# Kernel optimization log

Hardware: AMD Instinct MI355X
Metric: run time of the kernel (lower is better)

The kernel has to match this reference:

```python
import jax, jax.numpy as jnp
import numpy as np

B, T, D = 1024, 256, 256
H, L, K = 768, 6, 10          # hidden_dim, levels, conv_size
CH = H // L                   # chunk_size
GDIM = 4 * H + 2 * L          # gate projection width


def setup_inputs() -> dict:
    key = jax.random.key(0)
    ks = jax.random.split(key, 10)
    s = lambda n: 1.0 / np.sqrt(n).astype(np.float32)
    return {
        "x": jax.random.normal(ks[0], (B, T, D), jnp.float32),
        "time": jax.random.uniform(ks[1], (B, T), jnp.float32),
        "kernel_w": jax.random.normal(ks[2], (GDIM, D + 1), jnp.float32) * s(D + 1),
        "kernel_b": jnp.zeros((GDIM,), jnp.float32),
        "rec_w": jax.random.normal(ks[3], (GDIM, H + 1), jnp.float32) * s(H + 1),
        "rec_b": jnp.zeros((GDIM,), jnp.float32),
        "scale_w": jax.random.normal(ks[4], (H // 6, H), jnp.float32) * s(H),
        "scale_b": jnp.zeros((H // 6,), jnp.float32),
        "rescale_w": jax.random.normal(ks[5], (H, H // 6), jnp.float32) * s(H // 6),
        "rescale_b": jnp.zeros((H,), jnp.float32),
        "conv_w": jax.random.normal(ks[6], (H, H, K), jnp.float32) * s(H * K),
        "conv_b": jnp.zeros((H,), jnp.float32),
        "out_w": jax.random.normal(ks[7], (1, H), jnp.float32) * s(H),
        "out_b": jnp.zeros((1,), jnp.float32),
    }


def _cumax_l2r(v):
    return jnp.cumsum(jax.nn.softmax(v, axis=-1), axis=-1)


def _cumax_r2l(v):
    v = jnp.flip(v, -1)
    v = jnp.cumsum(jax.nn.softmax(v, axis=-1), axis=-1)
    return jnp.flip(v, -1)


def reference(x, time, kernel_w, kernel_b, rec_w, rec_b, scale_w, scale_b,
              rescale_w, rescale_b, conv_w, conv_b, out_w, out_b):
    b = x.shape[0]

    def step(carry, xs):
        c, h, tmp_h, tmp_dis = carry
        x_t, t_t = xs                              # [b,D], [b]
        xi = jnp.concatenate([x_t, t_t[:, None]], -1)
        hi = jnp.concatenate([h, t_t[:, None]], -1)
        g = xi @ kernel_w.T + kernel_b + hi @ rec_w.T + rec_b   # [b, 4H+2L]
        f_m = _cumax_l2r(g[:, :L])[:, :, None]                  # [b,L,1]
        i_m = _cumax_r2l(g[:, L:2 * L])[:, :, None]             # [b,L,1]
        rest = g[:, 2 * L:].reshape(b, 4 * L, CH)
        f_g = jax.nn.sigmoid(rest[:, :L])
        i_g = jax.nn.sigmoid(rest[:, L:2 * L])
        o_g = jax.nn.sigmoid(rest[:, 2 * L:3 * L])
        c_in = jnp.tanh(rest[:, 3 * L:])
        c_last = c.reshape(b, L, CH)
        ov = f_m * i_m
        c_new3 = ov * (f_g * c_last + i_g * c_in) + (f_m - ov) * c_last + (i_m - ov) * c_in
        h_new = (o_g * jnp.tanh(c_new3)).reshape(b, H)
        c_new = c_new3.reshape(b, H)
        dist = 1.0 - jnp.mean(f_m[..., 0], axis=-1)             # [b]
        tmp_h = jnp.concatenate([tmp_h[1:], h_new[None]], 0)    # sliding window [K,b,H]
        tmp_dis = jnp.concatenate([tmp_dis[1:], dist[None]], 0) # [K,b]
        return (c_new, h_new, tmp_h, tmp_dis), dist

    init = (jnp.zeros((b, H), x.dtype), jnp.zeros((b, H), x.dtype),
            jnp.zeros((K, b, H), x.dtype), jnp.zeros((K, b), x.dtype))
    xs = (jnp.transpose(x, (1, 0, 2)), time.T)
    (c_f, h_last, tmp_h, tmp_dis), distance = jax.lax.scan(step, init, xs)

    local_dis = jax.nn.softmax(jnp.cumsum(tmp_dis.T, axis=1), axis=1)    # [b,K]
    local_h = jnp.transpose(tmp_h, (1, 2, 0)) * local_dis[:, None, :]    # [b,H,K]
    theme = jax.nn.sigmoid(
        jax.nn.relu(jnp.mean(local_h, -1) @ scale_w.T + scale_b) @ rescale_w.T + rescale_b)
    conv = jnp.einsum('bhk,ohk->bo', local_h, conv_w) + conv_b           # Conv1d -> length-1 output
    rnn_out = theme * conv + h_last
    output = jax.nn.sigmoid((rnn_out @ out_w.T + out_b).reshape(b))
    return output, distance
```

## Files before the change

kernel.cpp:

```cpp
#include <hip/hip_runtime.h>
#include <hip/hip_bf16.h>
#include <math.h>
#include <stdint.h>

#define BATCH 1024
#define TT    256
#define DD    256
#define HH    768
#define LL    6
#define KCONV 10
#define CHW   128
#define KPACK 1024
#define G4    3072
#define BNT   192
#define GSTR  196

#define NSLOT   8
#define SLOT    17408
#define NS      (NSLOT * SLOT)
#define ML_OFF  52224
#define BIAS_OFF 139264
#define SMEM_SZ 140928

typedef __attribute__((ext_vector_type(8))) __bf16 bf16x8;
typedef __attribute__((ext_vector_type(4))) float f32x4;

__device__ __forceinline__ float sigf(float v) { return 1.0f / (1.0f + expf(-v)); }

#define SEL6(a, l) ((l)==0?a[0]:(l)==1?a[1]:(l)==2?a[2]:(l)==3?a[3]:(l)==4?a[4]:a[5])

__device__ __forceinline__ void gload16(const void* g, void* l) {
    __builtin_amdgcn_global_load_lds(
        (const __attribute__((address_space(1))) unsigned int*)g,
        (__attribute__((address_space(3))) unsigned int*)l, 16, 0, 0);
}
__device__ __forceinline__ void gload16_nc(const void* g, void* l) {
    __builtin_amdgcn_global_load_lds(
        (const __attribute__((address_space(1))) unsigned int*)g,
        (__attribute__((address_space(3))) unsigned int*)l, 16, 0, 0x11);
}

__device__ __forceinline__ unsigned short bf16bits(float v) {
    __hip_bfloat16 h(v);
    return *(unsigned short*)&h;
}

#define WAITV(a, b) do { \
    if (tid < 64) asm volatile("s_waitcnt vmcnt(" #a ")" ::: "memory"); \
    else          asm volatile("s_waitcnt vmcnt(" #b ")" ::: "memory"); \
} while (0)

__global__ __launch_bounds__(256) void prep_w4(
    const float* __restrict__ kw, const float* __restrict__ kb,
    const float* __restrict__ rw, const float* __restrict__ rb,
    __hip_bfloat16* __restrict__ W4, float* __restrict__ bias4, float* __restrict__ tco4)
{
    int n = blockIdx.x;
    int e = n >> 2, q = n & 3;
    int orig = 2 * LL + q * HH + e;
    int tid = threadIdx.x;
#pragma unroll
    for (int k = 0; k < 4; ++k) {
        int col = tid + k * 256;
        float v = (col < DD) ? kw[(size_t)orig * (DD + 1) + col]
                             : rw[(size_t)orig * (HH + 1) + (col - DD)];
        W4[(size_t)n * KPACK + col] = __hip_bfloat16(v);
    }
    if (tid == 0) {
        bias4[n] = kb[orig] + rb[orig];
        tco4[n]  = kw[(size_t)orig * (DD + 1) + DD] + rw[(size_t)orig * (HH + 1) + HH];
    }
}

__global__ __launch_bounds__(256) void prep_wm(
    const float* __restrict__ kw, const float* __restrict__ kb,
    const float* __restrict__ rw, const float* __restrict__ rb,
    __hip_bfloat16* __restrict__ Wm, float* __restrict__ mbias, float* __restrict__ mtco)
{
    int j = blockIdx.x;
    int tid = threadIdx.x;
#pragma unroll
    for (int k = 0; k < 4; ++k) {
        int col = tid + k * 256;
        float v = 0.0f;
        if (j < 12)
            v = (col < DD) ? kw[(size_t)j * (DD + 1) + col]
                           : rw[(size_t)j * (HH + 1) + (col - DD)];
        Wm[(size_t)j * KPACK + col] = __hip_bfloat16(v);
    }
    if (tid == 0 && j < 12) {
        mbias[j] = kb[j] + rb[j];
        mtco[j]  = kw[(size_t)j * (DD + 1) + DD] + rw[(size_t)j * (HH + 1) + HH];
    }
}

__global__ __launch_bounds__(256) void cvt_kernel(
    const float* __restrict__ src, __hip_bfloat16* __restrict__ dst, int n)
{
    int i = blockIdx.x * 256 + threadIdx.x;
    if (i < n) dst[i] = __hip_bfloat16(src[i]);
}

__global__ __launch_bounds__(256) void xcvt_kernel(
    const float* __restrict__ x, __hip_bfloat16* __restrict__ xb)
{
    size_t o = ((size_t)blockIdx.x * 256 + threadIdx.x) * 8;
    int t = (int)(o >> 18);
    int b = (int)(o >> 8) & 1023;
    int d = (int)(o & 255);
    const float* src = x + ((size_t)b * TT + t) * DD + d;
    float4 a = *(const float4*)src;
    float4 c = *(const float4*)(src + 4);
    unsigned short tmp[8];
    tmp[0] = bf16bits(a.x); tmp[1] = bf16bits(a.y);
    tmp[2] = bf16bits(a.z); tmp[3] = bf16bits(a.w);
    tmp[4] = bf16bits(c.x); tmp[5] = bf16bits(c.y);
    tmp[6] = bf16bits(c.z); tmp[7] = bf16bits(c.w);
    *(uint4*)((char*)xb + o * 2) = *(const uint4*)tmp;
}

__global__ __launch_bounds__(512, 1) void persist_kernel(
    __hip_bfloat16* __restrict__ Hb0,
    __hip_bfloat16* __restrict__ Hb1,
    const __hip_bfloat16* __restrict__ xb,
    const float* __restrict__ timep,
    const __hip_bfloat16* __restrict__ W4,
    const __hip_bfloat16* __restrict__ Wm,
    const float* __restrict__ bias4, const float* __restrict__ tco4,
    const float* __restrict__ mbias, const float* __restrict__ mtco,
    float* __restrict__ hwin,
    float* __restrict__ distp,
    unsigned* __restrict__ cnt)
{
    __shared__ __align__(16) char smem[SMEM_SZ];
    float* gl    = (float*)smem;
    float* ml    = (float*)(smem + ML_OFF);
    float* biasL = (float*)(smem + BIAS_OFF);
    float* tcoL  = biasL + 192;
    float* mbL   = tcoL + 192;
    float* mtL   = mbL + 16;

    const int tid = threadIdx.x;
    const int bid = blockIdx.x;
    const int swz = (bid & 7) * 32 + (bid >> 3);
    const int bm = swz & 15;
    const int bn = swz >> 4;

    const int lane = tid & 63;
    const int wid  = tid >> 6;
    const int wr   = wid >> 2, wc = wid & 3;
    const int kg   = lane >> 4;
    const int r15  = lane & 15;
    const bool domast = (wid == 3) || (wid == 4);
    const int r  = tid >> 3;
    const int qq = tid & 7;
    const int b  = bm * 64 + r;
    unsigned* cntg = cnt + bm * 64;

    if (tid < 192) { biasL[tid] = bias4[bn * BNT + tid]; tcoL[tid] = tco4[bn * BNT + tid]; }
    if (tid >= 256 && tid < 268) { mbL[tid - 256] = mbias[tid - 256]; mtL[tid - 256] = mtco[tid - 256]; }
    __syncthreads();

    float cst[6] = {0.f, 0.f, 0.f, 0.f, 0.f, 0.f};

    const int rowA = tid >> 2, kcA = tid & 3;
    const int swA  = kcA ^ ((rowA >> 1) & 3);
    const size_t aXoff = ((size_t)(bm * 64 + rowA) * DD + swA * 8) * 2;
    const size_t aHoff = ((size_t)(bm * 64 + rowA) * HH + swA * 8) * 2;
    const int aLds = tid * 16;
    auto bptr = [&](int cb) -> const char* {
        int row = cb >> 2, kc = cb & 3;
        int sw = kc ^ ((row >> 1) & 3);
        const __hip_bfloat16* src = (row < BNT)
            ? W4 + (size_t)(bn * BNT + row) * KPACK + sw * 8
            : Wm + (size_t)(row - BNT) * KPACK + sw * 8;
        return (const char*)src;
    };
    const char* bsrc0 = (tid >= 256) ? bptr(tid - 256) : (const char*)W4;
    const char* bsrc1 = bptr(tid + 256);
    const char* bsrc2 = (tid < 64) ? bptr(tid + 768) : (const char*)W4;
    const int bLds0 = 4096 + (tid - 256) * 16;
    const int bLds1 = 4096 + (tid + 256) * 16;
    const int bLds2 = 4096 + (tid + 768) * 16;

    int aOff[2], bOff[3];
#pragma unroll
    for (int m = 0; m < 2; ++m) {
        int ar = wr * 32 + m * 16 + r15;
        aOff[m] = (ar * 32 + ((kg ^ ((ar >> 1) & 3)) * 8)) * 2;
    }
#pragma unroll
    for (int n = 0; n < 3; ++n) {
        int br = wc * 48 + n * 16 + r15;
        bOff[n] = 4096 + (br * 32 + ((kg ^ ((br >> 1) & 3)) * 8)) * 2;
    }
    const int mrr = BNT + r15;
    const int mOff = 4096 + (mrr * 32 + ((kg ^ ((mrr >> 1) & 3)) * 8)) * 2;

    const char* hb0c = (const char*)Hb0;
    const char* hb1c = (const char*)Hb1;
    const char* xbt  = (const char*)xb;

    const char* pxA = xbt + aXoff;
    const char* phA = hb0c + aHoff;

    auto stage = [&](int slotOff, int tile) {
        const int toff = tile * 64;
        if (tid < 256) {
            if (tile < 8) gload16(pxA + toff, smem + slotOff + aLds);
            else          gload16_nc(phA + (toff - 512), smem + slotOff + aLds);
        } else {
            gload16(bsrc0 + toff, smem + slotOff + bLds0);
        }
        gload16(bsrc1 + toff, smem + slotOff + bLds1);
        if (tid < 64) gload16(bsrc2 + toff, smem + slotOff + bLds2);
    };

    stage(0 * SLOT, 0); stage(1 * SLOT, 1); stage(2 * SLOT, 2);
    stage(3 * SLOT, 3); stage(4 * SLOT, 4); stage(5 * SLOT, 5);

    for (int t = 0; t < TT; ++t) {
        const char* hbb = (t & 1) ? hb1c : hb0c;
        __hip_bfloat16* hbW = (t & 1) ? Hb0 : Hb1;
        phA = hbb + aHoff;

        f32x4 acc[2][3], accm[2];
#pragma unroll
        for (int m = 0; m < 2; ++m) {
#pragma unroll
            for (int n = 0; n < 3; ++n) acc[m][n] = (f32x4){0.f, 0.f, 0.f, 0.f};
            accm[m] = (f32x4){0.f, 0.f, 0.f, 0.f};
        }

        auto compute = [&](int slotOff) {
            const char* base = smem + slotOff;
            bf16x8 af[2], bv[3];
#pragma unroll
            for (int m = 0; m < 2; ++m) af[m] = *(const bf16x8*)(base + aOff[m]);
#pragma unroll
            for (int n = 0; n < 3; ++n) bv[n] = *(const bf16x8*)(base + bOff[n]);
#pragma unroll
            for (int m = 0; m < 2; ++m)
#pragma unroll
                for (int n = 0; n < 3; ++n)
                    acc[m][n] = __builtin_amdgcn_mfma_f32_16x16x32_bf16(
                        af[m], bv[n], acc[m][n], 0, 0, 0);
            if (domast) {
                bf16x8 bmf = *(const bf16x8*)(base + mOff);
#pragma unroll
                for (int m = 0; m < 2; ++m)
                    accm[m] = __builtin_amdgcn_mfma_f32_16x16x32_bf16(
                        af[m], bmf, accm[m], 0, 0, 0);
            }
        };

        int c0 = 0;
        int s0 = 6 * SLOT;
#pragma unroll 1
        for (int it = 0; it < 32; it += 2) {
            if (it <= 26)      WAITV(12, 8);
            else if (it == 28) WAITV(6, 4);
            else { asm volatile("s_waitcnt vmcnt(0)" ::: "memory"); }
            __builtin_amdgcn_s_barrier();
            int c1 = c0 + SLOT; if (c1 >= NS) c1 -= NS;
            if (it <= 24) {
                int s1 = s0 + SLOT; if (s1 >= NS) s1 -= NS;
                stage(s0, it + 6); stage(s1, it + 7);
                s0 = s1 + SLOT; if (s0 >= NS) s0 -= NS;
            }
            compute(c0); compute(c1);
            c0 = c1 + SLOT; if (c0 >= NS) c0 -= NS;
        }
        __syncthreads();

#pragma unroll
        for (int m = 0; m < 2; ++m)
#pragma unroll
            for (int n = 0; n < 3; ++n) {
                int col = wc * 48 + n * 16 + r15;
                int rw0 = wr * 32 + m * 16 + kg * 4;
#pragma unroll
                for (int j = 0; j < 4; ++j)
                    gl[(rw0 + j) * GSTR + col] = acc[m][n][j];
            }
        if (domast) {
#pragma unroll
            for (int m = 0; m < 2; ++m) {
                int rw0 = wr * 32 + m * 16 + kg * 4;
#pragma unroll
                for (int j = 0; j < 4; ++j)
                    ml[(rw0 + j) * 16 + r15] = accm[m][j];
            }
        }
        __syncthreads();

        const float tv = timep[(size_t)b * TT + t];

        float mv[12];
#pragma unroll
        for (int i2 = 0; i2 < 12; ++i2)
            mv[i2] = ml[r * 16 + i2] + mbL[i2] + tv * mtL[i2];

        float mxf = mv[0], mxi = mv[6];
#pragma unroll
        for (int i2 = 1; i2 < 6; ++i2) { mxf = fmaxf(mxf, mv[i2]); mxi = fmaxf(mxi, mv[6 + i2]); }
        float fr[6], ir[6];
        float sf = 0.f, si = 0.f;
#pragma unroll
        for (int i2 = 0; i2 < 6; ++i2) {
            fr[i2] = expf(mv[i2] - mxf);     sf += fr[i2];
            ir[i2] = expf(mv[6 + i2] - mxi); si += ir[i2];
        }
        float fm[6], im[6];
        float rsf = 1.0f / sf, rsi = 1.0f / si;
        fm[0] = fr[0] * rsf;
#pragma unroll
        for (int i2 = 1; i2 < 6; ++i2) fm[i2] = fm[i2 - 1] + fr[i2] * rsf;
        im[5] = ir[5] * rsi;
#pragma unroll
        for (int i2 = 4; i2 >= 0; --i2) im[i2] = im[i2 + 1] + ir[i2] * rsi;

        if (bn == 0 && qq == 0) {
            float dist = 1.0f - (fm[0] + fm[1] + fm[2] + fm[3] + fm[4] + fm[5]) * (1.0f / 6.0f);
            distp[(size_t)t * BATCH + b] = dist;
        }

        const int e0 = bn * 48 + qq * 6;
        const int l0 = e0 >> 7, l1 = (e0 + 5) >> 7;
        const float fmA = SEL6(fm, l0), imA = SEL6(im, l0);
        const float fmB = SEL6(fm, l1), imB = SEL6(im, l1);

        const bool wh = (t >= TT - KCONV);
        float* hw = hwin + (size_t)(t % KCONV) * BATCH * HH + (size_t)b * HH;

        unsigned short hsv[6];
#pragma unroll
        for (int j = 0; j < 6; ++j) {
            int el = qq * 6 + j;
            int e  = bn * 48 + el;
            f32x4 gv = *(const f32x4*)&gl[r * GSTR + el * 4];
            float fg = sigf(gv[0] + biasL[el * 4 + 0] + tv * tcoL[el * 4 + 0]);
            float ig = sigf(gv[1] + biasL[el * 4 + 1] + tv * tcoL[el * 4 + 1]);
            float og = sigf(gv[2] + biasL[el * 4 + 2] + tv * tcoL[el * 4 + 2]);
            float ci = tanhf(gv[3] + biasL[el * 4 + 3] + tv * tcoL[el * 4 + 3]);
            float cl = cst[j];
            bool hi = (e >> 7) != l0;
            float fmv = hi ? fmB : fmA;
            float imv = hi ? imB : imA;
            float ov = fmv * imv;
            float cn = ov * (fg * cl + ig * ci) + (fmv - ov) * cl + (imv - ov) * ci;
            float hn = og * tanhf(cn);
            cst[j] = cn;
            hsv[j] = bf16bits(hn);
            if (wh) hw[e] = hn;
        }
        {
            unsigned w0 = (unsigned)hsv[0] | ((unsigned)hsv[1] << 16);
            unsigned w1 = (unsigned)hsv[2] | ((unsigned)hsv[3] << 16);
            unsigned w2 = (unsigned)hsv[4] | ((unsigned)hsv[5] << 16);
            uint64_t ad = (uint64_t)(uintptr_t)(hbW + (size_t)b * HH + e0);
            asm volatile(
                "global_store_dword %0, %1, off sc0 sc1\n\t"
                "global_store_dword %0, %2, off offset:4 sc0 sc1\n\t"
                "global_store_dword %0, %3, off offset:8 sc0 sc1"
                :: "v"(ad), "v"(w0), "v"(w1), "v"(w2) : "memory");
        }
        __syncthreads();

        xbt += (size_t)BATCH * DD * 2;
        pxA = xbt + aXoff;
        if (t + 1 < TT) {
            asm volatile("s_waitcnt vmcnt(0)" ::: "memory");
            stage(0 * SLOT, 0); stage(1 * SLOT, 1); stage(2 * SLOT, 2);
            stage(3 * SLOT, 3); stage(4 * SLOT, 4); stage(5 * SLOT, 5);
            __builtin_amdgcn_s_barrier();
            if (tid == 0) {
                __hip_atomic_fetch_add(cntg, 1u, __ATOMIC_RELAXED, __HIP_MEMORY_SCOPE_AGENT);
                unsigned target = (unsigned)(t + 1) * 16u;
                while (__hip_atomic_load(cntg, __ATOMIC_RELAXED, __HIP_MEMORY_SCOPE_AGENT) < target)
                    __builtin_amdgcn_s_sleep(1);
            }
            __builtin_amdgcn_s_barrier();
        }
    }
}

template <int SPLIT>
__global__ __launch_bounds__(256, 2) void gemm_mfma(
    const __hip_bfloat16* __restrict__ A, int lda,
    const __hip_bfloat16* __restrict__ W, int ldw,
    float* __restrict__ C, int ldc, size_t cstride, int Kdim, int nbm, int nbn)
{
    __shared__ unsigned short As[2][64 * 64];
    __shared__ unsigned short Bs[2][128 * 64];

    const int nwg = nbm * nbn * SPLIT;
    const int cpx = nwg >> 3;
    const int bid = blockIdx.x;
    const int swz = (bid & 7) * cpx + (bid >> 3);
    const int z   = swz % SPLIT;
    const int t2  = swz / SPLIT;
    const int bm  = t2 % nbm;
    const int bn  = t2 / nbm;
    const int kspan = Kdim / SPLIT;

    const int tid  = threadIdx.x;
    const int lane = tid & 63;
    const int wid  = tid >> 6;
    const int wr   = wid >> 1, wc = wid & 1;
    const int kg   = lane >> 4;
    const int r15  = lane & 15;

    f32x4 acc[2][4];
#pragma unroll
    for (int m = 0; m < 2; ++m)
#pragma unroll
        for (int n = 0; n < 4; ++n) acc[m][n] = (f32x4){0.f, 0.f, 0.f, 0.f};

    const __hip_bfloat16* Abase = A + (size_t)(bm * 64) * lda + (size_t)z * kspan;
    const __hip_bfloat16* Wbase = W + (size_t)(bn * 128) * ldw + (size_t)z * kspan;

    auto stage = [&](int buf, int k0) {
        unsigned short* Ad = &As[buf][0];
        unsigned short* Bd = &Bs[buf][0];
#pragma unroll
        for (int i = 0; i < 2; ++i) {
            int c = tid + i * 256;
            int row = c >> 3, kc = c & 7;
            gload16(Abase + (size_t)row * lda + k0 + ((kc ^ (row & 7)) * 8), Ad + c * 8);
        }
#pragma unroll
        for (int i = 0; i < 4; ++i) {
            int c = tid + i * 256;
            int row = c >> 3, kc = c & 7;
            gload16(Wbase + (size_t)row * ldw + k0 + ((kc ^ (row & 7)) * 8), Bd + c * 8);
        }
    };

    const int NIT = kspan / 64;
    stage(0, 0);
    int cur = 0;
    for (int it = 0; it < NIT; ++it) {
        if (it + 1 < NIT) {
            stage(cur ^ 1, (it + 1) * 64);
            asm volatile("s_waitcnt vmcnt(6)" ::: "memory");
        } else {
            asm volatile("s_waitcnt vmcnt(0)" ::: "memory");
        }
        __builtin_amdgcn_s_barrier();

#pragma unroll
        for (int ks = 0; ks < 2; ++ks) {
            const int kb = ks * 4 + kg;
            bf16x8 af[2], bv[4];
#pragma unroll
            for (int m = 0; m < 2; ++m) {
                int ar = wr * 32 + m * 16 + r15;
                af[m] = *(const bf16x8*)&As[cur][ar * 64 + ((kb ^ (ar & 7)) * 8)];
            }
#pragma unroll
            for (int n = 0; n < 4; ++n) {
                int br = wc * 64 + n * 16 + r15;
                bv[n] = *(const bf16x8*)&Bs[cur][br * 64 + ((kb ^ (br & 7)) * 8)];
            }
#pragma unroll
            for (int m = 0; m < 2; ++m)
#pragma unroll
                for (int n = 0; n < 4; ++n)
                    acc[m][n] = __builtin_amdgcn_mfma_f32_16x16x32_bf16(
                        af[m], bv[n], acc[m][n], 0, 0, 0);
        }
        __builtin_amdgcn_s_barrier();
        cur ^= 1;
    }

    float* Cp = C + (size_t)z * cstride;
    const int crow0 = bm * 64 + wr * 32 + (lane >> 4) * 4;
    const int ccol0 = bn * 128 + wc * 64 + r15;
#pragma unroll
    for (int m = 0; m < 2; ++m)
#pragma unroll
        for (int n = 0; n < 4; ++n)
#pragma unroll
            for (int j = 0; j < 4; ++j)
                Cp[(size_t)(crow0 + m * 16 + j) * ldc + ccol0 + n * 16] = acc[m][n][j];
}

#define BM 64
#define BN 64
#define BK 32
template <int MODE>
__global__ __launch_bounds__(256) void gemm_nt(
    const float* __restrict__ A, int lda,
    const float* __restrict__ W, int ldw,
    const float* __restrict__ bias,
    float* __restrict__ C, int ldc, int M, int N, int Kdim)
{
    __shared__ float As[BK][BM + 4];
    __shared__ float Ws[BK][BN + 4];
    const int tid = threadIdx.x;
    const int bm = blockIdx.y * BM;
    const int bn = blockIdx.x * BN;
    const int tx = tid & 15;
    const int ty = tid >> 4;

    float acc[4][4];
#pragma unroll
    for (int i = 0; i < 4; ++i)
#pragma unroll
        for (int j = 0; j < 4; ++j) acc[i][j] = 0.0f;

    for (int k0 = 0; k0 < Kdim; k0 += BK) {
#pragma unroll
        for (int i = 0; i < (BM * BK) / 256; ++i) {
            int linear = tid + i * 256;
            int r = linear >> 5, kk = linear & 31;
            As[kk][r] = A[(size_t)(bm + r) * lda + k0 + kk];
        }
#pragma unroll
        for (int i = 0; i < (BN * BK) / 256; ++i) {
            int linear = tid + i * 256;
            int r = linear >> 5, kk = linear & 31;
            int gcol = bn + r;
            Ws[kk][r] = (gcol < N) ? W[(size_t)gcol * ldw + k0 + kk] : 0.0f;
        }
        __syncthreads();
#pragma unroll
        for (int kk = 0; kk < BK; ++kk) {
            float4 a4 = *(const float4*)&As[kk][ty * 4];
            float4 b4 = *(const float4*)&Ws[kk][tx * 4];
            float av[4] = {a4.x, a4.y, a4.z, a4.w};
            float bv[4] = {b4.x, b4.y, b4.z, b4.w};
#pragma unroll
            for (int i = 0; i < 4; ++i)
#pragma unroll
                for (int j = 0; j < 4; ++j)
                    acc[i][j] = fmaf(av[i], bv[j], acc[i][j]);
        }
        __syncthreads();
    }
#pragma unroll
    for (int i = 0; i < 4; ++i) {
        int row = bm + ty * 4 + i;
#pragma unroll
        for (int j = 0; j < 4; ++j) {
            int col = bn + tx * 4 + j;
            if (col < N) {
                float v = acc[i][j] + bias[col];
                if (MODE == 2) v = fmaxf(v, 0.0f);
                if (MODE == 3) v = sigf(v);
                C[(size_t)row * ldc + col] = v;
            }
        }
    }
}

__global__ __launch_bounds__(256) void window_kernel(
    const float* __restrict__ dist_out, float* __restrict__ ld)
{
    int b = blockIdx.x * blockDim.x + threadIdx.x;
    if (b >= BATCH) return;
    float w[KCONV];
    float run = 0.0f, m = -1e30f;
#pragma unroll
    for (int k = 0; k < KCONV; ++k) {
        run += dist_out[(size_t)(TT - KCONV + k) * BATCH + b];
        w[k] = run;
        m = fmaxf(m, run);
    }
    float s = 0.0f;
#pragma unroll
    for (int k = 0; k < KCONV; ++k) { w[k] = expf(w[k] - m); s += w[k]; }
    float inv = 1.0f / s;
#pragma unroll
    for (int k = 0; k < KCONV; ++k) ld[b * KCONV + k] = w[k] * inv;
}

__global__ __launch_bounds__(256) void localh_kernel(
    const float* __restrict__ hwin, const float* __restrict__ ld,
    __hip_bfloat16* __restrict__ Lhb, float* __restrict__ mh)
{
    int idx = blockIdx.x * 256 + threadIdx.x;
    int b = idx / HH;
    int e = idx - b * HH;
    float lv[KCONV];
#pragma unroll
    for (int k = 0; k < KCONV; ++k) lv[k] = ld[b * KCONV + k];
    float sum = 0.0f;
#pragma unroll
    for (int k = 0; k < KCONV; ++k) {
        int slot = (TT - KCONV + k) % KCONV;
        float v = hwin[(size_t)slot * BATCH * HH + (size_t)b * HH + e] * lv[k];
        Lhb[(size_t)b * (HH * KCONV) + e * KCONV + k] = __hip_bfloat16(v);
        sum += v;
    }
    mh[idx] = sum * (1.0f / KCONV);
}

__global__ __launch_bounds__(256) void out_kernel(
    const float* __restrict__ theme, const float* __restrict__ convp, size_t cstride,
    const float* __restrict__ conv_b, const float* __restrict__ hbuf,
    const float* __restrict__ out_w, const float* __restrict__ out_b,
    float* __restrict__ out)
{
    __shared__ float red[256];
    int b = blockIdx.x;
    float p = 0.0f;
    for (int e = threadIdx.x; e < HH; e += 256) {
        float cv = conv_b[e];
#pragma unroll
        for (int zz = 0; zz < 2; ++zz)
            cv += convp[(size_t)zz * cstride + (size_t)b * HH + e];
        p += (theme[(size_t)b * HH + e] * cv + hbuf[(size_t)b * HH + e]) * out_w[e];
    }
    red[threadIdx.x] = p;
    __syncthreads();
    for (int s = 128; s > 0; s >>= 1) {
        if (threadIdx.x < s) red[threadIdx.x] += red[threadIdx.x + s];
        __syncthreads();
    }
    if (threadIdx.x == 0) out[b] = sigf(red[0] + out_b[0]);
}

extern "C" void kernel_launch(void* const* d_in, const int* in_sizes, int n_in,
                              void* d_out, int out_size, void* d_ws, size_t ws_size,
                              hipStream_t stream)
{
    const float* x       = (const float*)d_in[0];
    const float* timep   = (const float*)d_in[1];
    const float* kw      = (const float*)d_in[2];
    const float* kb      = (const float*)d_in[3];
    const float* rw      = (const float*)d_in[4];
    const float* rb      = (const float*)d_in[5];
    const float* scale_w = (const float*)d_in[6];
    const float* scale_b = (const float*)d_in[7];
    const float* resc_w  = (const float*)d_in[8];
    const float* resc_b  = (const float*)d_in[9];
    const float* conv_w  = (const float*)d_in[10];
    const float* conv_b  = (const float*)d_in[11];
    const float* out_w   = (const float*)d_in[12];
    const float* out_b   = (const float*)d_in[13];

    float* outp  = (float*)d_out;
    float* distp = outp + BATCH;

    char* cur = (char*)d_ws;
    auto carve = [&](size_t bytes) {
        char* p = cur;
        cur += (bytes + 255) & ~(size_t)255;
        return (void*)p;
    };
    __hip_bfloat16* W4     = (__hip_bfloat16*)carve((size_t)G4 * KPACK * 2);
    __hip_bfloat16* Wm     = (__hip_bfloat16*)carve((size_t)16 * KPACK * 2);
    __hip_bfloat16* xb     = (__hip_bfloat16*)carve((size_t)TT * BATCH * DD * 2);
    __hip_bfloat16* Hb0    = (__hip_bfloat16*)carve((size_t)BATCH * HH * 2);
    __hip_bfloat16* Hb1    = (__hip_bfloat16*)carve((size_t)BATCH * HH * 2);
    __hip_bfloat16* Lhb    = (__hip_bfloat16*)carve((size_t)BATCH * HH * KCONV * 2);
    __hip_bfloat16* convwb = (__hip_bfloat16*)carve((size_t)HH * HH * KCONV * 2);
    float* bias4 = (float*)carve(G4 * 4);
    float* tco4  = (float*)carve(G4 * 4);
    float* mbias = (float*)carve(64);
    float* mtco  = (float*)carve(64);
    unsigned* cnt = (unsigned*)carve(4096);
    float* hwin  = (float*)carve((size_t)KCONV * BATCH * HH * 4);
    float* ld    = (float*)carve((size_t)BATCH * KCONV * 4);
    float* mh    = (float*)carve((size_t)BATCH * HH * 4);
    float* s1    = (float*)carve((size_t)BATCH * CHW * 4);
    float* theme = (float*)carve((size_t)BATCH * HH * 4);
    float* convp = (float*)carve(2 * (size_t)BATCH * HH * 4);

    hipMemsetAsync(cnt, 0, 4096, stream);
    hipMemsetAsync(Hb0, 0, (size_t)BATCH * HH * 2, stream);
    prep_w4<<<G4, 256, 0, stream>>>(kw, kb, rw, rb, W4, bias4, tco4);
    prep_wm<<<16, 256, 0, stream>>>(kw, kb, rw, rb, Wm, mbias, mtco);
    cvt_kernel<<<(HH * HH * KCONV + 255) / 256, 256, 0, stream>>>(
        conv_w, convwb, HH * HH * KCONV);
    xcvt_kernel<<<(TT * BATCH * DD / 8 + 255) / 256, 256, 0, stream>>>(x, xb);

    {
        void* args[] = {
            (void*)&Hb0, (void*)&Hb1, (void*)&xb, (void*)&timep,
            (void*)&W4, (void*)&Wm, (void*)&bias4, (void*)&tco4,
            (void*)&mbias, (void*)&mtco, (void*)&hwin, (void*)&distp,
            (void*)&cnt
        };
        hipLaunchCooperativeKernel((void*)persist_kernel, dim3(256), dim3(512),
                                   args, 0, stream);
    }

    window_kernel<<<(BATCH + 255) / 256, 256, 0, stream>>>(distp, ld);
    localh_kernel<<<(BATCH * HH) / 256, 256, 0, stream>>>(hwin, ld, Lhb, mh);

    gemm_mfma<2><<<16 * 6 * 2, 256, 0, stream>>>(
        Lhb, HH * KCONV, convwb, HH * KCONV, convp, HH, (size_t)BATCH * HH,
        HH * KCONV, 16, 6);
    gemm_nt<2><<<dim3(CHW / BN, BATCH / BM), 256, 0, stream>>>(
        mh, HH, scale_w, HH, scale_b, s1, CHW, BATCH, CHW, HH);
    gemm_nt<3><<<dim3(HH / BN, BATCH / BM), 256, 0, stream>>>(
        s1, CHW, resc_w, CHW, resc_b, theme, HH, BATCH, HH, CHW);

    out_kernel<<<BATCH, 256, 0, stream>>>(
        theme, convp, (size_t)BATCH * HH, conv_b,
        hwin + (size_t)((TT - 1) % KCONV) * BATCH * HH,
        out_w, out_b, outp);
}
```

Before: 4.804 ms.

## Double persistent kernel block to 1024 threads with 16-row wave tiles

The persistent recurrent kernel now launches 1024 threads per block instead of 512. Each wave's MFMA tile is cut from 32x48 to 16x48. The B-tile staging loads are redistributed over the extra threads, and the element-wise gate update handles 3 hidden units per thread instead of 6. The aim is more waves to hide load and LDS latency and to shorten the serial per-step gate phase. The cost is less operand reuse per wave, more LDS reads per MFMA, and unaligned dword-plus-short stores of the hidden state.

```diff
diff --git a/kernel.cpp b/kernel.cpp
--- a/kernel.cpp
+++ b/kernel.cpp
@@ -119,7 +119,7 @@
     *(uint4*)((char*)xb + o * 2) = *(const uint4*)tmp;
 }
 
-__global__ __launch_bounds__(512, 1) void persist_kernel(
+__global__ __launch_bounds__(1024, 1) void persist_kernel(
     __hip_bfloat16* __restrict__ Hb0,
     __hip_bfloat16* __restrict__ Hb1,
     const __hip_bfloat16* __restrict__ xb,
@@ -148,20 +148,20 @@
 
     const int lane = tid & 63;
     const int wid  = tid >> 6;
-    const int wr   = wid >> 2, wc = wid & 3;
+    const int wr   = wid & 3, wc = wid >> 2;
     const int kg   = lane >> 4;
     const int r15  = lane & 15;
-    const bool domast = (wid == 3) || (wid == 4);
-    const int r  = tid >> 3;
-    const int qq = tid & 7;
-    const int b  = bm * 64 + r;
+    const bool domast = (wc == 3);
+    const int r   = tid >> 4;
+    const int q16 = tid & 15;
+    const int b   = bm * 64 + r;
     unsigned* cntg = cnt + bm * 64;
 
     if (tid < 192) { biasL[tid] = bias4[bn * BNT + tid]; tcoL[tid] = tco4[bn * BNT + tid]; }
     if (tid >= 256 && tid < 268) { mbL[tid - 256] = mbias[tid - 256]; mtL[tid - 256] = mtco[tid - 256]; }
     __syncthreads();
 
-    float cst[6] = {0.f, 0.f, 0.f, 0.f, 0.f, 0.f};
+    float cst[3] = {0.f, 0.f, 0.f};
 
     const int rowA = tid >> 2, kcA = tid & 3;
     const int swA  = kcA ^ ((rowA >> 1) & 3);
@@ -177,17 +177,14 @@
         return (const char*)src;
     };
     const char* bsrc0 = (tid >= 256) ? bptr(tid - 256) : (const char*)W4;
-    const char* bsrc1 = bptr(tid + 256);
     const char* bsrc2 = (tid < 64) ? bptr(tid + 768) : (const char*)W4;
     const int bLds0 = 4096 + (tid - 256) * 16;
-    const int bLds1 = 4096 + (tid + 256) * 16;
     const int bLds2 = 4096 + (tid + 768) * 16;
 
-    int aOff[2], bOff[3];
-#pragma unroll
-    for (int m = 0; m < 2; ++m) {
-        int ar = wr * 32 + m * 16 + r15;
-        aOff[m] = (ar * 32 + ((kg ^ ((ar >> 1) & 3)) * 8)) * 2;
+    int aOff, bOff[3];
+    {
+        int ar = wr * 16 + r15;
+        aOff = (ar * 32 + ((kg ^ ((ar >> 1) & 3)) * 8)) * 2;
     }
 #pragma unroll
     for (int n = 0; n < 3; ++n) {
@@ -212,7 +209,6 @@
         } else {
             gload16(bsrc0 + toff, smem + slotOff + bLds0);
         }
-        gload16(bsrc1 + toff, smem + slotOff + bLds1);
         if (tid < 64) gload16(bsrc2 + toff, smem + slotOff + bLds2);
     };
 
@@ -224,33 +220,25 @@
         __hip_bfloat16* hbW = (t & 1) ? Hb0 : Hb1;
         phA = hbb + aHoff;
 
-        f32x4 acc[2][3], accm[2];
-#pragma unroll
-        for (int m = 0; m < 2; ++m) {
-#pragma unroll
-            for (int n = 0; n < 3; ++n) acc[m][n] = (f32x4){0.f, 0.f, 0.f, 0.f};
-            accm[m] = (f32x4){0.f, 0.f, 0.f, 0.f};
-        }
+        f32x4 acc[3], accm;
+#pragma unroll
+        for (int n = 0; n < 3; ++n) acc[n] = (f32x4){0.f, 0.f, 0.f, 0.f};
+        accm = (f32x4){0.f, 0.f, 0.f, 0.f};
 
         auto compute = [&](int slotOff) {
             const char* base = smem + slotOff;
-            bf16x8 af[2], bv[3];
-#pragma unroll
-            for (int m = 0; m < 2; ++m) af[m] = *(const bf16x8*)(base + aOff[m]);
+            bf16x8 af = *(const bf16x8*)(base + aOff);
+            bf16x8 bv[3];
 #pragma unroll
             for (int n = 0; n < 3; ++n) bv[n] = *(const bf16x8*)(base + bOff[n]);
 #pragma unroll
-            for (int m = 0; m < 2; ++m)
-#pragma unroll
-                for (int n = 0; n < 3; ++n)
-                    acc[m][n] = __builtin_amdgcn_mfma_f32_16x16x32_bf16(
-                        af[m], bv[n], acc[m][n], 0, 0, 0);
+            for (int n = 0; n < 3; ++n)
+                acc[n] = __builtin_amdgcn_mfma_f32_16x16x32_bf16(
+                    af, bv[n], acc[n], 0, 0, 0);
             if (domast) {
                 bf16x8 bmf = *(const bf16x8*)(base + mOff);
-#pragma unroll
-                for (int m = 0; m < 2; ++m)
-                    accm[m] = __builtin_amdgcn_mfma_f32_16x16x32_bf16(
-                        af[m], bmf, accm[m], 0, 0, 0);
+                accm = __builtin_amdgcn_mfma_f32_16x16x32_bf16(
+                    af, bmf, accm, 0, 0, 0);
             }
         };
 
@@ -258,8 +246,8 @@
         int s0 = 6 * SLOT;
 #pragma unroll 1
         for (int it = 0; it < 32; it += 2) {
-            if (it <= 26)      WAITV(12, 8);
-            else if (it == 28) WAITV(6, 4);
+            if (it <= 26)      WAITV(8, 4);
+            else if (it == 28) WAITV(4, 2);
             else { asm volatile("s_waitcnt vmcnt(0)" ::: "memory"); }
             __builtin_amdgcn_s_barrier();
             int c1 = c0 + SLOT; if (c1 >= NS) c1 -= NS;
@@ -274,23 +262,18 @@
         __syncthreads();
 
 #pragma unroll
-        for (int m = 0; m < 2; ++m)
-#pragma unroll
-            for (int n = 0; n < 3; ++n) {
-                int col = wc * 48 + n * 16 + r15;
-                int rw0 = wr * 32 + m * 16 + kg * 4;
-#pragma unroll
-                for (int j = 0; j < 4; ++j)
-                    gl[(rw0 + j) * GSTR + col] = acc[m][n][j];
-            }
+        for (int n = 0; n < 3; ++n) {
+            int col = wc * 48 + n * 16 + r15;
+            int rw0 = wr * 16 + kg * 4;
+#pragma unroll
+            for (int j = 0; j < 4; ++j)
+                gl[(rw0 + j) * GSTR + col] = acc[n][j];
+        }
         if (domast) {
-#pragma unroll
-            for (int m = 0; m < 2; ++m) {
-                int rw0 = wr * 32 + m * 16 + kg * 4;
-#pragma unroll
-                for (int j = 0; j < 4; ++j)
-                    ml[(rw0 + j) * 16 + r15] = accm[m][j];
-            }
+            int rw0 = wr * 16 + kg * 4;
+#pragma unroll
+            for (int j = 0; j < 4; ++j)
+                ml[(rw0 + j) * 16 + r15] = accm[j];
         }
         __syncthreads();
 
@@ -320,23 +303,23 @@
 #pragma unroll
         for (int i2 = 4; i2 >= 0; --i2) im[i2] = im[i2 + 1] + ir[i2] * rsi;
 
-        if (bn == 0 && qq == 0) {
+        if (bn == 0 && q16 == 0) {
             float dist = 1.0f - (fm[0] + fm[1] + fm[2] + fm[3] + fm[4] + fm[5]) * (1.0f / 6.0f);
             distp[(size_t)t * BATCH + b] = dist;
         }
 
-        const int e0 = bn * 48 + qq * 6;
-        const int l0 = e0 >> 7, l1 = (e0 + 5) >> 7;
+        const int e0 = bn * 48 + q16 * 3;
+        const int l0 = e0 >> 7, l1 = (e0 + 2) >> 7;
         const float fmA = SEL6(fm, l0), imA = SEL6(im, l0);
         const float fmB = SEL6(fm, l1), imB = SEL6(im, l1);
 
         const bool wh = (t >= TT - KCONV);
         float* hw = hwin + (size_t)(t % KCONV) * BATCH * HH + (size_t)b * HH;
 
-        unsigned short hsv[6];
-#pragma unroll
-        for (int j = 0; j < 6; ++j) {
-            int el = qq * 6 + j;
+        unsigned short hsv[3];
+#pragma unroll
+        for (int j = 0; j < 3; ++j) {
+            int el = q16 * 3 + j;
             int e  = bn * 48 + el;
             f32x4 gv = *(const f32x4*)&gl[r * GSTR + el * 4];
             float fg = sigf(gv[0] + biasL[el * 4 + 0] + tv * tcoL[el * 4 + 0]);
@@ -356,14 +339,12 @@
         }
         {
             unsigned w0 = (unsigned)hsv[0] | ((unsigned)hsv[1] << 16);
-            unsigned w1 = (unsigned)hsv[2] | ((unsigned)hsv[3] << 16);
-            unsigned w2 = (unsigned)hsv[4] | ((unsigned)hsv[5] << 16);
+            unsigned w1 = (unsigned)hsv[2];
             uint64_t ad = (uint64_t)(uintptr_t)(hbW + (size_t)b * HH + e0);
             asm volatile(
                 "global_store_dword %0, %1, off sc0 sc1\n\t"
-                "global_store_dword %0, %2, off offset:4 sc0 sc1\n\t"
-                "global_store_dword %0, %3, off offset:8 sc0 sc1"
-                :: "v"(ad), "v"(w0), "v"(w1), "v"(w2) : "memory");
+                "global_store_short %0, %2, off offset:4 sc0 sc1"
+                :: "v"(ad), "v"(w0), "v"(w1) : "memory");
         }
         __syncthreads();
 
@@ -684,7 +665,7 @@
             (void*)&mbias, (void*)&mtco, (void*)&hwin, (void*)&distp,
             (void*)&cnt
         };
-        hipLaunchCooperativeKernel((void*)persist_kernel, dim3(256), dim3(512),
+        hipLaunchCooperativeKernel((void*)persist_kernel, dim3(256), dim3(1024),
                                    args, 0, stream);
     }
 
```

Result: no change. 4.789 ms (-0.3%).
